# Performance work log

Measured on AMD Instinct MI355X. Metric: run time of the kernel, lower is better.

The kernel has to match this reference:

```python
import jax, jax.numpy as jnp
import numpy as np

B = 4096
DIM = 2048
B1 = 25   # root children (level-2 inner nodes)
B2 = 40   # leaves per level-2 node
NUM_CLASSES = B1 * B2  # 1000


def setup_inputs() -> dict:
    key = jax.random.key(0)
    k1, k2, k3, k4 = jax.random.split(key, 4)
    x = jax.random.normal(k1, (B, DIM), dtype=jnp.float32)
    labels = jax.random.randint(k2, (B,), 0, NUM_CLASSES, dtype=jnp.int64)
    # per-node Linear(dim, num_child + 1); column 0 = 'not in subtree'
    W_root = jax.random.normal(k3, (DIM, B1 + 1), dtype=jnp.float32) * 0.02
    b_root = jnp.zeros((B1 + 1,), dtype=jnp.float32)
    W_lvl2 = jax.random.normal(k4, (B1, DIM, B2 + 1), dtype=jnp.float32) * 0.02
    b_lvl2 = jnp.zeros((B1, B2 + 1), dtype=jnp.float32)
    return {"x": x, "labels": labels, "W_root": W_root, "b_root": b_root,
            "W_lvl2": W_lvl2, "b_lvl2": b_lvl2}


def reference(x, labels, W_root, b_root, W_lvl2, b_lvl2):
    b = x.shape[0]
    b1 = W_lvl2.shape[0]
    b2 = W_lvl2.shape[2] - 1

    # layer 1: root classifier (root.path_prob == 1.0)
    root_logits = x @ W_root + b_root                       # [B, b1+1]
    root_lp = jax.nn.log_softmax(root_logits, axis=-1)
    root_prob = jnp.exp(root_lp)

    # layer 2: all level-2 node classifiers as one grouped GEMM
    lvl2_logits = jnp.einsum('bd,ndk->bnk', x, W_lvl2) + b_lvl2  # [B, b1, b2+1]
    lvl2_lp = jax.nn.log_softmax(lvl2_logits, axis=-1)
    lvl2_prob = jnp.exp(lvl2_lp)

    # leaf path_prob = P(child under node n) * P(node n under root);
    # leaves tile out columns contiguously (label2id of complete tree)
    out = (lvl2_prob[:, :, 1:] * root_prob[:, 1:, None]).reshape(b, b1 * b2)

    # penalty: CE at each inner node divided by its layer l
    j = labels // b2                                        # level-2 parent index
    i = labels % b2                                         # leaf index within parent
    ce_root = -jnp.take_along_axis(root_lp, (j + 1)[:, None], axis=1).mean()
    # sub-label for node n: i+1 if label's parent is n, else 0
    sub_lab = jnp.where(j[:, None] == jnp.arange(b1)[None, :], (i + 1)[:, None], 0)
    gathered = jnp.take_along_axis(lvl2_lp, sub_lab[:, :, None], axis=2)[..., 0]  # [B, b1]
    penalty = ce_root + (-gathered).mean(axis=0).sum() / 2.0

    return out, penalty
```

## Files before the change

### kernel.cpp

```cpp
#include <hip/hip_runtime.h>
#include <stdint.h>

#define TB 256

typedef __bf16 bf16x8 __attribute__((ext_vector_type(8)));
typedef float f32x4 __attribute__((ext_vector_type(4)));

#define AS1 __attribute__((address_space(1)))
#define AS3 __attribute__((address_space(3)))
#define GLOAD16(gp, lp) __builtin_amdgcn_global_load_lds( \
    (const AS1 unsigned int*)(gp), (AS3 unsigned int*)(lp), 16, 0, 0)

__device__ __forceinline__ unsigned short f2bf(float f) {
  uint32_t u = __builtin_bit_cast(uint32_t, f);
  u += 0x7fffu + ((u >> 16) & 1u);
  return (unsigned short)(u >> 16);
}

__device__ __forceinline__ void waitbar3() {
  __builtin_amdgcn_sched_barrier(0);
  asm volatile("s_waitcnt vmcnt(3) lgkmcnt(0)" ::: "memory");
  __builtin_amdgcn_s_barrier();
  __builtin_amdgcn_sched_barrier(0);
}
__device__ __forceinline__ void waitbar0() {
  __builtin_amdgcn_sched_barrier(0);
  asm volatile("s_waitcnt vmcnt(0) lgkmcnt(0)" ::: "memory");
  __builtin_amdgcn_s_barrier();
  __builtin_amdgcn_sched_barrier(0);
}

__global__ __launch_bounds__(TB) void k_prep(const float* __restrict__ x,
                                             const float* __restrict__ wl,
                                             const float* __restrict__ wr,
                                             const int* __restrict__ labraw,
                                             unsigned short* __restrict__ xbf,
                                             unsigned short* __restrict__ wlt,
                                             unsigned short* __restrict__ wrt,
                                             int* __restrict__ lab32,
                                             float* __restrict__ pengl) {
  int bid = blockIdx.x, t = threadIdx.x;
  if (bid < 4096) {
    int idx = bid * TB + t;
    const float4* xin = reinterpret_cast<const float4*>(x);
    float4 a = xin[idx * 2], b = xin[idx * 2 + 1];
    uint32_t p0 = f2bf(a.x) | ((uint32_t)f2bf(a.y) << 16);
    uint32_t p1 = f2bf(a.z) | ((uint32_t)f2bf(a.w) << 16);
    uint32_t p2 = f2bf(b.x) | ((uint32_t)f2bf(b.y) << 16);
    uint32_t p3 = f2bf(b.z) | ((uint32_t)f2bf(b.w) << 16);
    reinterpret_cast<uint4*>(xbf)[idx] = make_uint4(p0, p1, p2, p3);
  } else if (bid < 4928) {
    __shared__ float ld_f[2624];
    int b2 = bid - 4096;
    if (b2 < 800) {
      int n = b2 / 32, dt = b2 % 32, d0 = dt * 64;
      const float* src = wl + ((size_t)n * 2048 + d0) * 41;
      for (int i = 0; i < 11; i++) { int lin = t + TB * i; if (lin < 2624) ld_f[lin] = src[lin]; }
      __syncthreads();
      unsigned short* dst = wlt + (size_t)n * 48 * 2048 + d0;
      for (int i = 0; i < 12; i++) {
        int lin = t + TB * i;
        int wc = lin >> 6, d = lin & 63;
        float v = (wc < 41) ? ld_f[d * 41 + wc] : 0.f;
        dst[(size_t)wc * 2048 + d] = f2bf(v);
      }
    } else {
      int dt = b2 - 800, d0 = dt * 64;
      const float* src = wr + (size_t)d0 * 26;
      for (int i = 0; i < 7; i++) { int lin = t + TB * i; if (lin < 1664) ld_f[lin] = src[lin]; }
      __syncthreads();
      unsigned short* dst = wrt + d0;
      for (int i = 0; i < 8; i++) {
        int lin = t + TB * i;
        int wc = lin >> 6, d = lin & 63;
        float v = (wc < 26) ? ld_f[d * 26 + wc] : 0.f;
        dst[(size_t)wc * 2048 + d] = f2bf(v);
      }
    }
  } else if (bid == 4928) {
    __shared__ int orred;
    if (t == 0) { orred = 0; pengl[0] = 0.f; }
    __syncthreads();
    int acc = 0;
    for (int i = t; i < 2048; i += TB) acc |= labraw[2 * i + 1];
    atomicOr(&orred, acc);
    __syncthreads();
    bool i64 = (orred == 0);
    for (int i = t; i < 4096; i += TB) lab32[i] = i64 ? labraw[2 * i] : labraw[i];
  } else {
    int g = 25 + (bid - 4929);
    uint4* p = reinterpret_cast<uint4*>(wlt + (size_t)g * 48 * 2048);
    uint4 z = make_uint4(0, 0, 0, 0);
    for (int i = t; i < 12288; i += TB) p[i] = z;
  }
}

__global__ __launch_bounds__(512) void k_root(const unsigned short* __restrict__ xbf,
                                              const unsigned short* __restrict__ wrt,
                                              const float* __restrict__ br,
                                              const int* __restrict__ labels,
                                              float* __restrict__ rootp,
                                              float* __restrict__ pengl) {
  __shared__ __align__(16) unsigned char lds3[3][24576];
  int r0 = blockIdx.x * 16;
  int tid = threadIdx.x, lane = tid & 63, wave = tid >> 6;
  int lq = lane >> 4, lr = lane & 15;
  const unsigned short* xg = xbf + (size_t)r0 * 2048;
  f32x4 acc[2] = {};

#define STAGE_RT(lb, kk)                                                              \
  do {                                                                                \
    {                                                    \
      int row = tid >> 5, s = tid & 31;                                               \
      const unsigned short* gp = xg + (size_t)row * 2048 + (kk) + ((s ^ row) << 3);   \
      GLOAD16(gp, (lb) + (size_t)tid * 16);                                           \
    }                                                                                 \
    _Pragma("unroll")                                                                 \
    for (int i = 0; i < 2; i++) {                       \
      int idx = i * 512 + tid;                                                        \
      int wc = idx >> 5, s = idx & 31;                                                \
      const unsigned short* gp = wrt + (size_t)wc * 2048 + (kk) + ((s ^ (wc & 31)) << 3); \
      GLOAD16(gp, (lb) + 8192 + (size_t)idx * 16);                                    \
    }                                                                                 \
  } while (0)

#define COMPUTE_RT(base)                                                              \
  do {                                                                                \
    int g = (wave << 2) | lq;                      \
    bf16x8 af[2], bx;                                                                 \
    _Pragma("unroll")                                                                 \
    for (int mt = 0; mt < 2; mt++) {                                                  \
      int c = mt * 16 + lr;                                                           \
      af[mt] = *reinterpret_cast<const bf16x8*>((base) + 8192 + c * 512 + ((g ^ (c & 31)) << 4)); \
    }                                                                                 \
    bx = *reinterpret_cast<const bf16x8*>((base) + lr * 512 + ((g ^ lr) << 4));       \
    _Pragma("unroll")                                                                 \
    for (int mt = 0; mt < 2; mt++)                                                    \
      acc[mt] = __builtin_amdgcn_mfma_f32_16x16x32_bf16(af[mt], bx, acc[mt], 0, 0, 0); \
  } while (0)

  STAGE_RT(&lds3[0][0], 0);
  STAGE_RT(&lds3[1][0], 256);
  waitbar3();
  int cur = 0;
#pragma unroll 3
  for (int t = 0; t < 6; ++t) {
    int nx = cur + 2; if (nx >= 3) nx -= 3;
    STAGE_RT(&lds3[nx][0], (t + 2) * 256);
    COMPUTE_RT(&lds3[cur][0]);
    waitbar3();
    ++cur; if (cur == 3) cur = 0;
  }
  COMPUTE_RT(&lds3[cur][0]);
  waitbar0();
  ++cur; if (cur == 3) cur = 0;
  COMPUTE_RT(&lds3[cur][0]);
  __syncthreads();

  float* red = (float*)&lds3[0][0];
  int li = (wave * 64 + lane) * 8;
#pragma unroll
  for (int mt = 0; mt < 2; mt++)
#pragma unroll
    for (int r = 0; r < 4; r++) red[li + mt * 4 + r] = acc[mt][r];
  __syncthreads();
  if (wave == 0) {
    float lg[2][4];
    float m = -1e30f;
#pragma unroll
    for (int mt = 0; mt < 2; mt++)
#pragma unroll
      for (int r = 0; r < 4; r++) {
        float v = 0.f;
#pragma unroll
        for (int w = 0; w < 8; w++) v += red[(w * 64 + lane) * 8 + mt * 4 + r];
        int wc = mt * 16 + lq * 4 + r;
        v += (wc < 26) ? br[wc] : -1e30f;
        lg[mt][r] = v;
        m = fmaxf(m, v);
      }
    m = fmaxf(m, __shfl_xor(m, 16));
    m = fmaxf(m, __shfl_xor(m, 32));
    float s = 0.f;
#pragma unroll
    for (int mt = 0; mt < 2; mt++)
#pragma unroll
      for (int r = 0; r < 4; r++) s += expf(lg[mt][r] - m);
    s += __shfl_xor(s, 16);
    s += __shfl_xor(s, 32);
    float ls = logf(s);
    int b = r0 + lr;
    int lab = labels[b];
    int j = lab / 40;
    float pen = 0.f;
#pragma unroll
    for (int mt = 0; mt < 2; mt++)
#pragma unroll
      for (int r = 0; r < 4; r++) {
        int wc = mt * 16 + lq * 4 + r;
        float lp = lg[mt][r] - m - ls;
        if (wc < 26) rootp[(size_t)b * 32 + wc] = expf(lp);
        if (wc == j + 1) pen -= lp;
      }
    for (int off = 32; off; off >>= 1) pen += __shfl_down(pen, off);
    if (lane == 0) atomicAdd(pengl, pen * (1.f / 4096.f));
  }
}

__global__ __launch_bounds__(TB, 2) void k_lvl2(const unsigned short* __restrict__ xbf,
                                                const unsigned short* __restrict__ wlt,
                                                const float* __restrict__ bl,
                                                const int* __restrict__ labels,
                                                const float* __restrict__ rootp,
                                                float* __restrict__ out,
                                                float* __restrict__ pengl) {
  __shared__ __align__(16) unsigned char ldsb[2][40960];
  int bid = blockIdx.x;
  int swz = (bid & 7) * 28 + (bid >> 3);
  int rt = swz / 7, quad = swz % 7;
  int r0 = rt * 128, n0 = quad * 4;
  int tid = threadIdx.x, lane = tid & 63, wave = tid >> 6;
  int wr = wave >> 1, wc = wave & 1;
  int lq = lane >> 4, lr = lane & 15;
  f32x4 acc[6][4] = {};
  const unsigned short* xg = xbf + (size_t)r0 * 2048;
  const unsigned short* wg = wlt + (size_t)n0 * 48 * 2048;

#define STAGE_L2(lb, kk)                                                              \
  do {                                                                                \
    _Pragma("unroll")                                                                 \
    for (int i = 0; i < 4; i++) {                      \
      int idx = i * 256 + tid;                                                        \
      int row = idx >> 3, s = idx & 7;                                                \
      const unsigned short* gp = xg + (size_t)row * 2048 + (kk) + ((s ^ (row & 7)) << 3); \
      GLOAD16(gp, (lb) + (size_t)idx * 16);                                           \
    }                                                                                 \
    _Pragma("unroll")                                                                 \
    for (int i = 0; i < 6; i++) {                      \
      int idx = i * 256 + tid;                                                        \
      int wrow = idx >> 3, s = idx & 7;                                               \
      const unsigned short* gp = wg + (size_t)wrow * 2048 + (kk) + ((s ^ (wrow & 7)) << 3); \
      GLOAD16(gp, (lb) + 16384 + (size_t)idx * 16);                                   \
    }                                                                                 \
  } while (0)

#define COMPUTE_L2(base)                                                              \
  do {                                                                                \
    _Pragma("unroll")                                                                 \
    for (int ks = 0; ks < 2; ks++) {                                                  \
      int g = (ks << 2) | lq;                                                         \
      bf16x8 af[6], bx[4];                                                            \
      _Pragma("unroll")                                                               \
      for (int mt = 0; mt < 6; mt++) {                                                \
        int c = wc * 96 + mt * 16 + lr;                                               \
        af[mt] = *reinterpret_cast<const bf16x8*>((base) + 16384 + c * 128 + ((g ^ (c & 7)) << 4)); \
      }                                                                               \
      _Pragma("unroll")                                                               \
      for (int nt = 0; nt < 4; nt++) {                                                \
        int row = wr * 64 + nt * 16 + lr;                                             \
        bx[nt] = *reinterpret_cast<const bf16x8*>((base) + row * 128 + ((g ^ (row & 7)) << 4)); \
      }                                                                               \
      _Pragma("unroll")                                                               \
      for (int mt = 0; mt < 6; mt++)                                                  \
        _Pragma("unroll")                                                             \
        for (int nt = 0; nt < 4; nt++)                                                \
          acc[mt][nt] = __builtin_amdgcn_mfma_f32_16x16x32_bf16(af[mt], bx[nt], acc[mt][nt], 0, 0, 0); \
    }                                                                                 \
  } while (0)

  STAGE_L2(&ldsb[0][0], 0);
  __syncthreads();
#pragma unroll 2
  for (int t = 0; t < 32; ++t) {
    if (t < 31) STAGE_L2(&ldsb[(t + 1) & 1][0], (t + 1) * 64);
    COMPUTE_L2(&ldsb[t & 1][0]);
    __syncthreads();
  }

  float pen = 0.f;
#pragma unroll
  for (int gi = 0; gi < 2; gi++) {
    int n = n0 + 2 * wc + gi;
    bool valid = (n < 25);
    float bb[3][4];
#pragma unroll
    for (int q = 0; q < 3; q++)
#pragma unroll
      for (int r = 0; r < 4; r++) {
        int wcg = q * 16 + lq * 4 + r;
        bb[q][r] = (valid && wcg < 41) ? bl[n * 41 + wcg] : -1e30f;
      }
#pragma unroll
    for (int nt = 0; nt < 4; nt++) {
      int b = r0 + wr * 64 + nt * 16 + lr;
      float lg[3][4];
      float m = -1e30f;
#pragma unroll
      for (int q = 0; q < 3; q++)
#pragma unroll
        for (int r = 0; r < 4; r++) {
          float v = acc[gi * 3 + q][nt][r] + bb[q][r];
          lg[q][r] = v;
          m = fmaxf(m, v);
        }
      m = fmaxf(m, __shfl_xor(m, 16));
      m = fmaxf(m, __shfl_xor(m, 32));
      float s = 0.f;
#pragma unroll
      for (int q = 0; q < 3; q++)
#pragma unroll
        for (int r = 0; r < 4; r++) s += expf(lg[q][r] - m);
      s += __shfl_xor(s, 16);
      s += __shfl_xor(s, 32);
      float ls = logf(s);
      float rp = valid ? rootp[(size_t)b * 32 + (n + 1)] : 0.f;
      int lab = labels[b];
      int j = lab / 40;
      int sub = (j == n) ? (lab - j * 40 + 1) : 0;
#pragma unroll
      for (int q = 0; q < 3; q++)
#pragma unroll
        for (int r = 0; r < 4; r++) {
          int wcg = q * 16 + lq * 4 + r;
          float lp = lg[q][r] - m - ls;
          if (valid && wcg >= 1 && wcg < 41) out[(size_t)b * 1000 + n * 40 + wcg - 1] = expf(lp) * rp;
          if (valid && wcg == sub) pen -= lp;
        }
    }
  }
  for (int off = 32; off; off >>= 1) pen += __shfl_down(pen, off);
  float* red = (float*)&ldsb[0][0];
  if (lane == 0) red[wave] = pen;
  __syncthreads();
  if (tid == 0) atomicAdd(pengl, (red[0] + red[1] + red[2] + red[3]) * (1.f / 8192.f));
}

extern "C" void kernel_launch(void* const* d_in, const int* in_sizes, int n_in,
                              void* d_out, int out_size, void* d_ws, size_t ws_size,
                              hipStream_t stream) {
  const float* x = (const float*)d_in[0];
  const int* labels_raw = (const int*)d_in[1];
  const float* wroot = (const float*)d_in[2];
  const float* broot = (const float*)d_in[3];
  const float* wlvl2 = (const float*)d_in[4];
  const float* blvl2 = (const float*)d_in[5];
  float* out = (float*)d_out;
  float* pengl = out + 4096000;

  char* ws = (char*)d_ws;
  unsigned short* xbf = (unsigned short*)ws;
  unsigned short* wlt = (unsigned short*)(ws + 16777216);
  unsigned short* wrt = (unsigned short*)(ws + 22282240);
  float* rootp = (float*)(ws + 22413312);
  int* lab32 = (int*)(ws + 22937600);

  k_prep<<<4932, TB, 0, stream>>>(x, wlvl2, wroot, labels_raw, xbf, wlt, wrt, lab32, pengl);
  k_root<<<256, 512, 0, stream>>>(xbf, wrt, broot, lab32, rootp, pengl);
  k_lvl2<<<224, TB, 0, stream>>>(xbf, wlt, blvl2, lab32, rootp, out, pengl);
}
```

Measured before the change: 159.1 us.

## Pre-swizzle operands into MFMA fragment layout and load directly to registers

The prep kernel now writes x and both weight sets in a fragment-major bf16 layout, so each MFMA lane's 8-element operand is a contiguous 16-byte load. The root and level-2 GEMM kernels drop LDS staging and barriers and instead load fragments straight from global memory into registers with a double-buffered register pipeline. Level-2 becomes 832 single-wave blocks, each with a 96x64 tile. This removes LDS traffic and synchronisation, at the cost of no cross-wave data sharing, so operand reuse now depends on L2 cache and register pressure is high.

```diff
diff --git a/kernel.cpp b/kernel.cpp
--- a/kernel.cpp
+++ b/kernel.cpp
@@ -5,79 +5,94 @@
 
 typedef __bf16 bf16x8 __attribute__((ext_vector_type(8)));
 typedef float f32x4 __attribute__((ext_vector_type(4)));
-
-#define AS1 __attribute__((address_space(1)))
-#define AS3 __attribute__((address_space(3)))
-#define GLOAD16(gp, lp) __builtin_amdgcn_global_load_lds( \
-    (const AS1 unsigned int*)(gp), (AS3 unsigned int*)(lp), 16, 0, 0)
 
 __device__ __forceinline__ unsigned short f2bf(float f) {
   uint32_t u = __builtin_bit_cast(uint32_t, f);
   u += 0x7fffu + ((u >> 16) & 1u);
   return (unsigned short)(u >> 16);
 }
-
-__device__ __forceinline__ void waitbar3() {
-  __builtin_amdgcn_sched_barrier(0);
-  asm volatile("s_waitcnt vmcnt(3) lgkmcnt(0)" ::: "memory");
-  __builtin_amdgcn_s_barrier();
-  __builtin_amdgcn_sched_barrier(0);
-}
-__device__ __forceinline__ void waitbar0() {
-  __builtin_amdgcn_sched_barrier(0);
-  asm volatile("s_waitcnt vmcnt(0) lgkmcnt(0)" ::: "memory");
-  __builtin_amdgcn_s_barrier();
-  __builtin_amdgcn_sched_barrier(0);
-}
+__device__ __forceinline__ uint32_t pk2(float a, float b) {
+  return (uint32_t)f2bf(a) | ((uint32_t)f2bf(b) << 16);
+}
+
+#define LD8(p) (*reinterpret_cast<const bf16x8*>(p))
+
 
 __global__ __launch_bounds__(TB) void k_prep(const float* __restrict__ x,
                                              const float* __restrict__ wl,
                                              const float* __restrict__ wr,
                                              const int* __restrict__ labraw,
-                                             unsigned short* __restrict__ xbf,
-                                             unsigned short* __restrict__ wlt,
-                                             unsigned short* __restrict__ wrt,
+                                             unsigned short* __restrict__ xf,
+                                             unsigned short* __restrict__ wf,
                                              int* __restrict__ lab32,
                                              float* __restrict__ pengl) {
+  __shared__ float ld[64 * 67];
   int bid = blockIdx.x, t = threadIdx.x;
-  if (bid < 4096) {
-    int idx = bid * TB + t;
-    const float4* xin = reinterpret_cast<const float4*>(x);
-    float4 a = xin[idx * 2], b = xin[idx * 2 + 1];
-    uint32_t p0 = f2bf(a.x) | ((uint32_t)f2bf(a.y) << 16);
-    uint32_t p1 = f2bf(a.z) | ((uint32_t)f2bf(a.w) << 16);
-    uint32_t p2 = f2bf(b.x) | ((uint32_t)f2bf(b.y) << 16);
-    uint32_t p3 = f2bf(b.z) | ((uint32_t)f2bf(b.w) << 16);
-    reinterpret_cast<uint4*>(xbf)[idx] = make_uint4(p0, p1, p2, p3);
-  } else if (bid < 4928) {
-    __shared__ float ld_f[2624];
-    int b2 = bid - 4096;
-    if (b2 < 800) {
-      int n = b2 / 32, dt = b2 % 32, d0 = dt * 64;
-      const float* src = wl + ((size_t)n * 2048 + d0) * 41;
-      for (int i = 0; i < 11; i++) { int lin = t + TB * i; if (lin < 2624) ld_f[lin] = src[lin]; }
-      __syncthreads();
-      unsigned short* dst = wlt + (size_t)n * 48 * 2048 + d0;
-      for (int i = 0; i < 12; i++) {
-        int lin = t + TB * i;
-        int wc = lin >> 6, d = lin & 63;
-        float v = (wc < 41) ? ld_f[d * 41 + wc] : 0.f;
-        dst[(size_t)wc * 2048 + d] = f2bf(v);
-      }
-    } else {
-      int dt = b2 - 800, d0 = dt * 64;
-      const float* src = wr + (size_t)d0 * 26;
-      for (int i = 0; i < 7; i++) { int lin = t + TB * i; if (lin < 1664) ld_f[lin] = src[lin]; }
-      __syncthreads();
-      unsigned short* dst = wrt + d0;
-      for (int i = 0; i < 8; i++) {
-        int lin = t + TB * i;
-        int wc = lin >> 6, d = lin & 63;
-        float v = (wc < 26) ? ld_f[d * 26 + wc] : 0.f;
-        dst[(size_t)wc * 2048 + d] = f2bf(v);
-      }
-    }
-  } else if (bid == 4928) {
+  if (bid < 2048) {
+    int rb = bid >> 5, kstep = bid & 31;
+    int r0 = rb * 64, k0 = kstep * 64;
+#pragma unroll
+    for (int u = 0; u < 4; u++) {
+      int ft = u * 256 + t;
+      int i = ft >> 4, j4 = ft & 15;
+      float4 v = *reinterpret_cast<const float4*>(x + (size_t)(r0 + i) * 2048 + k0 + j4 * 4);
+      ld[i * 67 + j4 * 4 + 0] = v.x; ld[i * 67 + j4 * 4 + 1] = v.y;
+      ld[i * 67 + j4 * 4 + 2] = v.z; ld[i * 67 + j4 * 4 + 3] = v.w;
+    }
+    __syncthreads();
+#pragma unroll
+    for (int u = 0; u < 2; u++) {
+      int c = u * 256 + t;
+      int subR = c >> 7, ks = (c >> 6) & 1, lane = c & 63;
+      int row = subR * 16 + (lane & 15);
+      int kl = ks * 32 + (lane >> 4) * 8;
+      const float* s = &ld[row * 67 + kl];
+      uint4 o = make_uint4(pk2(s[0], s[1]), pk2(s[2], s[3]), pk2(s[4], s[5]), pk2(s[6], s[7]));
+      size_t R = rb * 4 + subR;
+      *reinterpret_cast<uint4*>(xf + ((R * 32 + kstep) * 2 + ks) * 512 + lane * 8) = o;
+    }
+  } else if (bid < 2848) {
+    int b2 = bid - 2048;
+    int n = b2 >> 5, kstep = b2 & 31;
+    const float* src = wl + ((size_t)n * 2048 + kstep * 64) * 41;
+    for (int u = 0; u < 11; u++) { int lin = t + TB * u; if (lin < 2624) ld[lin] = src[lin]; }
+    __syncthreads();
+#pragma unroll
+    for (int u = 0; u < 2; u++) {
+      int c = u * 256 + t;
+      if (c < 384) {
+        int cq = c >> 7, ks = (c >> 6) & 1, lane = c & 63;
+        int col = cq * 16 + (lane & 15);
+        int kl = ks * 32 + (lane >> 4) * 8;
+        float v[8];
+#pragma unroll
+        for (int j = 0; j < 8; j++) v[j] = (col < 41) ? ld[(kl + j) * 41 + col] : 0.f;
+        uint4 o = make_uint4(pk2(v[0], v[1]), pk2(v[2], v[3]), pk2(v[4], v[5]), pk2(v[6], v[7]));
+        size_t C = n * 3 + cq;
+        *reinterpret_cast<uint4*>(wf + ((C * 32 + kstep) * 2 + ks) * 512 + lane * 8) = o;
+      }
+    }
+  } else if (bid < 2880) {
+    int kstep = bid - 2848;
+    const float* src = wr + (size_t)kstep * 64 * 26;
+    for (int u = 0; u < 7; u++) { int lin = t + TB * u; if (lin < 1664) ld[lin] = src[lin]; }
+    __syncthreads();
+#pragma unroll
+    for (int u = 0; u < 2; u++) {
+      int c = u * 256 + t;
+      if (c < 384) {
+        int cq = c >> 7, ks = (c >> 6) & 1, lane = c & 63;
+        int col = cq * 16 + (lane & 15);
+        int kl = ks * 32 + (lane >> 4) * 8;
+        float v[8];
+#pragma unroll
+        for (int j = 0; j < 8; j++) v[j] = (col < 26) ? ld[(kl + j) * 26 + col] : 0.f;
+        uint4 o = make_uint4(pk2(v[0], v[1]), pk2(v[2], v[3]), pk2(v[4], v[5]), pk2(v[6], v[7]));
+        size_t C = 75 + cq;
+        *reinterpret_cast<uint4*>(wf + ((C * 32 + kstep) * 2 + ks) * 512 + lane * 8) = o;
+      }
+    }
+  } else {
     __shared__ int orred;
     if (t == 0) { orred = 0; pengl[0] = 0.f; }
     __syncthreads();
@@ -87,77 +102,44 @@
     __syncthreads();
     bool i64 = (orred == 0);
     for (int i = t; i < 4096; i += TB) lab32[i] = i64 ? labraw[2 * i] : labraw[i];
-  } else {
-    int g = 25 + (bid - 4929);
-    uint4* p = reinterpret_cast<uint4*>(wlt + (size_t)g * 48 * 2048);
-    uint4 z = make_uint4(0, 0, 0, 0);
-    for (int i = t; i < 12288; i += TB) p[i] = z;
-  }
-}
-
-__global__ __launch_bounds__(512) void k_root(const unsigned short* __restrict__ xbf,
-                                              const unsigned short* __restrict__ wrt,
-                                              const float* __restrict__ br,
-                                              const int* __restrict__ labels,
-                                              float* __restrict__ rootp,
-                                              float* __restrict__ pengl) {
-  __shared__ __align__(16) unsigned char lds3[3][24576];
-  int r0 = blockIdx.x * 16;
+  }
+}
+
+__global__ __launch_bounds__(TB) void k_root(const unsigned short* __restrict__ xf,
+                                             const unsigned short* __restrict__ wf,
+                                             const float* __restrict__ br,
+                                             const int* __restrict__ labels,
+                                             float* __restrict__ rootp,
+                                             float* __restrict__ pengl) {
+  __shared__ float red[4 * 64 * 8];
+  int bid = blockIdx.x;
   int tid = threadIdx.x, lane = tid & 63, wave = tid >> 6;
   int lq = lane >> 4, lr = lane & 15;
-  const unsigned short* xg = xbf + (size_t)r0 * 2048;
   f32x4 acc[2] = {};
-
-#define STAGE_RT(lb, kk)                                                              \
-  do {                                                                                \
-    {                                                    \
-      int row = tid >> 5, s = tid & 31;                                               \
-      const unsigned short* gp = xg + (size_t)row * 2048 + (kk) + ((s ^ row) << 3);   \
-      GLOAD16(gp, (lb) + (size_t)tid * 16);                                           \
-    }                                                                                 \
-    _Pragma("unroll")                                                                 \
-    for (int i = 0; i < 2; i++) {                       \
-      int idx = i * 512 + tid;                                                        \
-      int wc = idx >> 5, s = idx & 31;                                                \
-      const unsigned short* gp = wrt + (size_t)wc * 2048 + (kk) + ((s ^ (wc & 31)) << 3); \
-      GLOAD16(gp, (lb) + 8192 + (size_t)idx * 16);                                    \
-    }                                                                                 \
-  } while (0)
-
-#define COMPUTE_RT(base)                                                              \
-  do {                                                                                \
-    int g = (wave << 2) | lq;                      \
-    bf16x8 af[2], bx;                                                                 \
-    _Pragma("unroll")                                                                 \
-    for (int mt = 0; mt < 2; mt++) {                                                  \
-      int c = mt * 16 + lr;                                                           \
-      af[mt] = *reinterpret_cast<const bf16x8*>((base) + 8192 + c * 512 + ((g ^ (c & 31)) << 4)); \
-    }                                                                                 \
-    bx = *reinterpret_cast<const bf16x8*>((base) + lr * 512 + ((g ^ lr) << 4));       \
-    _Pragma("unroll")                                                                 \
-    for (int mt = 0; mt < 2; mt++)                                                    \
-      acc[mt] = __builtin_amdgcn_mfma_f32_16x16x32_bf16(af[mt], bx, acc[mt], 0, 0, 0); \
-  } while (0)
-
-  STAGE_RT(&lds3[0][0], 0);
-  STAGE_RT(&lds3[1][0], 256);
-  waitbar3();
-  int cur = 0;
-#pragma unroll 3
-  for (int t = 0; t < 6; ++t) {
-    int nx = cur + 2; if (nx >= 3) nx -= 3;
-    STAGE_RT(&lds3[nx][0], (t + 2) * 256);
-    COMPUTE_RT(&lds3[cur][0]);
-    waitbar3();
-    ++cur; if (cur == 3) cur = 0;
-  }
-  COMPUTE_RT(&lds3[cur][0]);
-  waitbar0();
-  ++cur; if (cur == 3) cur = 0;
-  COMPUTE_RT(&lds3[cur][0]);
-  __syncthreads();
-
-  float* red = (float*)&lds3[0][0];
+  const unsigned short* xb = xf + (size_t)bid * 32768 + lane * 8;
+  const unsigned short* w0 = wf + (size_t)75 * 32768 + lane * 8;
+  const unsigned short* w1 = wf + (size_t)76 * 32768 + lane * 8;
+  int kb0 = wave * 8 * 1024;
+
+#define RLOAD(W, X, kb)                                                  \
+  do { _Pragma("unroll") for (int ks = 0; ks < 2; ks++) {                \
+      W[ks][0] = LD8(w0 + (kb) + ks * 512);                              \
+      W[ks][1] = LD8(w1 + (kb) + ks * 512);                              \
+      X[ks] = LD8(xb + (kb) + ks * 512); } } while (0)
+#define RMFMA(W, X)                                                      \
+  do { _Pragma("unroll") for (int ks = 0; ks < 2; ks++)                  \
+      _Pragma("unroll") for (int mt = 0; mt < 2; mt++)                   \
+        acc[mt] = __builtin_amdgcn_mfma_f32_16x16x32_bf16(W[ks][mt], X[ks], acc[mt], 0, 0, 0); } while (0)
+
+  bf16x8 A[2][2], Xa[2], B[2][2], Xb[2];
+  RLOAD(A, Xa, kb0);
+#pragma unroll
+  for (int tt = 0; tt < 3; ++tt) {
+    RLOAD(B, Xb, kb0 + (2 * tt + 1) * 1024); RMFMA(A, Xa);
+    RLOAD(A, Xa, kb0 + (2 * tt + 2) * 1024); RMFMA(B, Xb);
+  }
+  RLOAD(B, Xb, kb0 + 7 * 1024); RMFMA(A, Xa); RMFMA(B, Xb);
+
   int li = (wave * 64 + lane) * 8;
 #pragma unroll
   for (int mt = 0; mt < 2; mt++)
@@ -173,7 +155,7 @@
       for (int r = 0; r < 4; r++) {
         float v = 0.f;
 #pragma unroll
-        for (int w = 0; w < 8; w++) v += red[(w * 64 + lane) * 8 + mt * 4 + r];
+        for (int w = 0; w < 4; w++) v += red[(w * 64 + lane) * 8 + mt * 4 + r];
         int wc = mt * 16 + lq * 4 + r;
         v += (wc < 26) ? br[wc] : -1e30f;
         lg[mt][r] = v;
@@ -189,7 +171,7 @@
     s += __shfl_xor(s, 16);
     s += __shfl_xor(s, 32);
     float ls = logf(s);
-    int b = r0 + lr;
+    int b = bid * 16 + lr;
     int lab = labels[b];
     int j = lab / 40;
     float pen = 0.f;
@@ -207,80 +189,56 @@
   }
 }
 
-__global__ __launch_bounds__(TB, 2) void k_lvl2(const unsigned short* __restrict__ xbf,
-                                                const unsigned short* __restrict__ wlt,
-                                                const float* __restrict__ bl,
-                                                const int* __restrict__ labels,
-                                                const float* __restrict__ rootp,
-                                                float* __restrict__ out,
-                                                float* __restrict__ pengl) {
-  __shared__ __align__(16) unsigned char ldsb[2][40960];
+__global__ __launch_bounds__(64) void k_lvl2(const unsigned short* __restrict__ xf,
+                                             const unsigned short* __restrict__ wf,
+                                             const float* __restrict__ bl,
+                                             const int* __restrict__ labels,
+                                             const float* __restrict__ rootp,
+                                             float* __restrict__ out,
+                                             float* __restrict__ pengl) {
   int bid = blockIdx.x;
-  int swz = (bid & 7) * 28 + (bid >> 3);
-  int rt = swz / 7, quad = swz % 7;
-  int r0 = rt * 128, n0 = quad * 4;
-  int tid = threadIdx.x, lane = tid & 63, wave = tid >> 6;
-  int wr = wave >> 1, wc = wave & 1;
+  int swz = (bid & 7) * 104 + (bid >> 3);
+  int wcb = swz / 64, rt = swz % 64;
+  int lane = threadIdx.x;
   int lq = lane >> 4, lr = lane & 15;
   f32x4 acc[6][4] = {};
-  const unsigned short* xg = xbf + (size_t)r0 * 2048;
-  const unsigned short* wg = wlt + (size_t)n0 * 48 * 2048;
-
-#define STAGE_L2(lb, kk)                                                              \
-  do {                                                                                \
-    _Pragma("unroll")                                                                 \
-    for (int i = 0; i < 4; i++) {                      \
-      int idx = i * 256 + tid;                                                        \
-      int row = idx >> 3, s = idx & 7;                                                \
-      const unsigned short* gp = xg + (size_t)row * 2048 + (kk) + ((s ^ (row & 7)) << 3); \
-      GLOAD16(gp, (lb) + (size_t)idx * 16);                                           \
-    }                                                                                 \
-    _Pragma("unroll")                                                                 \
-    for (int i = 0; i < 6; i++) {                      \
-      int idx = i * 256 + tid;                                                        \
-      int wrow = idx >> 3, s = idx & 7;                                               \
-      const unsigned short* gp = wg + (size_t)wrow * 2048 + (kk) + ((s ^ (wrow & 7)) << 3); \
-      GLOAD16(gp, (lb) + 16384 + (size_t)idx * 16);                                   \
-    }                                                                                 \
-  } while (0)
-
-#define COMPUTE_L2(base)                                                              \
-  do {                                                                                \
-    _Pragma("unroll")                                                                 \
-    for (int ks = 0; ks < 2; ks++) {                                                  \
-      int g = (ks << 2) | lq;                                                         \
-      bf16x8 af[6], bx[4];                                                            \
-      _Pragma("unroll")                                                               \
-      for (int mt = 0; mt < 6; mt++) {                                                \
-        int c = wc * 96 + mt * 16 + lr;                                               \
-        af[mt] = *reinterpret_cast<const bf16x8*>((base) + 16384 + c * 128 + ((g ^ (c & 7)) << 4)); \
-      }                                                                               \
-      _Pragma("unroll")                                                               \
-      for (int nt = 0; nt < 4; nt++) {                                                \
-        int row = wr * 64 + nt * 16 + lr;                                             \
-        bx[nt] = *reinterpret_cast<const bf16x8*>((base) + row * 128 + ((g ^ (row & 7)) << 4)); \
-      }                                                                               \
-      _Pragma("unroll")                                                               \
-      for (int mt = 0; mt < 6; mt++)                                                  \
-        _Pragma("unroll")                                                             \
-        for (int nt = 0; nt < 4; nt++)                                                \
-          acc[mt][nt] = __builtin_amdgcn_mfma_f32_16x16x32_bf16(af[mt], bx[nt], acc[mt][nt], 0, 0, 0); \
-    }                                                                                 \
-  } while (0)
-
-  STAGE_L2(&ldsb[0][0], 0);
-  __syncthreads();
-#pragma unroll 2
-  for (int t = 0; t < 32; ++t) {
-    if (t < 31) STAGE_L2(&ldsb[(t + 1) & 1][0], (t + 1) * 64);
-    COMPUTE_L2(&ldsb[t & 1][0]);
-    __syncthreads();
-  }
-
+  const unsigned short* wb[6];
+  const unsigned short* xb[4];
+#pragma unroll
+  for (int c = 0; c < 6; c++) wb[c] = wf + (size_t)(wcb * 6 + c) * 32768 + lane * 8;
+#pragma unroll
+  for (int nt = 0; nt < 4; nt++) xb[nt] = xf + (size_t)(rt * 4 + nt) * 32768 + lane * 8;
+
+#define LLOAD(W, X, kb)                                                  \
+  do { _Pragma("unroll") for (int ks = 0; ks < 2; ks++) {                \
+      _Pragma("unroll") for (int c = 0; c < 6; c++)                      \
+        W[ks][c] = LD8(wb[c] + (kb) + ks * 512);                         \
+      _Pragma("unroll") for (int nt = 0; nt < 4; nt++)                   \
+        X[ks][nt] = LD8(xb[nt] + (kb) + ks * 512); } } while (0)
+#define LMFMA(W, X)                                                      \
+  do { _Pragma("unroll") for (int ks = 0; ks < 2; ks++)                  \
+      _Pragma("unroll") for (int mt = 0; mt < 6; mt++)                   \
+        _Pragma("unroll") for (int nt = 0; nt < 4; nt++)                 \
+          acc[mt][nt] = __builtin_amdgcn_mfma_f32_16x16x32_bf16(W[ks][mt], X[ks][nt], acc[mt][nt], 0, 0, 0); } while (0)
+
+  bf16x8 A[2][6], Xa[2][4], B[2][6], Xb[2][4];
+  LLOAD(A, Xa, 0);
+#pragma unroll 1
+  for (int tt = 0; tt < 15; ++tt) {
+    LLOAD(B, Xb, (2 * tt + 1) * 1024);
+    LMFMA(A, Xa);
+    LLOAD(A, Xa, (2 * tt + 2) * 1024);
+    LMFMA(B, Xb);
+  }
+  LLOAD(B, Xb, 31 * 1024);
+  LMFMA(A, Xa);
+  LMFMA(B, Xb);
+
+  int b0 = rt * 64;
   float pen = 0.f;
 #pragma unroll
   for (int gi = 0; gi < 2; gi++) {
-    int n = n0 + 2 * wc + gi;
+    int n = wcb * 2 + gi;
     bool valid = (n < 25);
     float bb[3][4];
 #pragma unroll
@@ -292,7 +250,7 @@
       }
 #pragma unroll
     for (int nt = 0; nt < 4; nt++) {
-      int b = r0 + wr * 64 + nt * 16 + lr;
+      int b = b0 + nt * 16 + lr;
       float lg[3][4];
       float m = -1e30f;
 #pragma unroll
@@ -329,10 +287,7 @@
     }
   }
   for (int off = 32; off; off >>= 1) pen += __shfl_down(pen, off);
-  float* red = (float*)&ldsb[0][0];
-  if (lane == 0) red[wave] = pen;
-  __syncthreads();
-  if (tid == 0) atomicAdd(pengl, (red[0] + red[1] + red[2] + red[3]) * (1.f / 8192.f));
+  if (lane == 0) atomicAdd(pengl, pen * (1.f / 8192.f));
 }
 
 extern "C" void kernel_launch(void* const* d_in, const int* in_sizes, int n_in,
@@ -348,13 +303,12 @@
   float* pengl = out + 4096000;
 
   char* ws = (char*)d_ws;
-  unsigned short* xbf = (unsigned short*)ws;
-  unsigned short* wlt = (unsigned short*)(ws + 16777216);
-  unsigned short* wrt = (unsigned short*)(ws + 22282240);
-  float* rootp = (float*)(ws + 22413312);
-  int* lab32 = (int*)(ws + 22937600);
-
-  k_prep<<<4932, TB, 0, stream>>>(x, wlvl2, wroot, labels_raw, xbf, wlt, wrt, lab32, pengl);
-  k_root<<<256, 512, 0, stream>>>(xbf, wrt, broot, lab32, rootp, pengl);
-  k_lvl2<<<224, TB, 0, stream>>>(xbf, wlt, blvl2, lab32, rootp, out, pengl);
-}
+  unsigned short* xf = (unsigned short*)ws;
+  unsigned short* wf = (unsigned short*)(ws + 16777216);
+  float* rootp = (float*)(ws + 21889024);
+  int* lab32 = (int*)(ws + 22413312);
+
+  k_prep<<<2881, TB, 0, stream>>>(x, wlvl2, wroot, labels_raw, xf, wf, lab32, pengl);
+  k_root<<<256, TB, 0, stream>>>(xf, wf, broot, lab32, rootp, pengl);
+  k_lvl2<<<832, 64, 0, stream>>>(xf, wf, blvl2, lab32, rootp, out, pengl);
+}
```

After: 174.7 us. 9.8% more time.

## Merge root and level-2 GEMMs into one split-K GEMM with separate epilogue

Applied to the files above, without the earlier changes.

Packs the root weights into the same transposed bf16 weight buffer as the level-2 weights, making one 4096x1280 GEMM. It runs as 640 blocks of 128x128 tiles with a two-way K split that writes fp32 partials to workspace. A separate epilogue kernel sums the partials and computes both log-softmaxes, the output probabilities and the penalty. This removes the separate root kernel and its rootp round trip and raises block count for occupancy. In exchange it adds about 42MB of partial writes and reads, drops the double-buffered LDS pipelining, and runs the epilogue with one thread per row-node over scalar loops.

```diff
diff --git a/kernel.cpp b/kernel.cpp
--- a/kernel.cpp
+++ b/kernel.cpp
@@ -15,19 +15,6 @@
   uint32_t u = __builtin_bit_cast(uint32_t, f);
   u += 0x7fffu + ((u >> 16) & 1u);
   return (unsigned short)(u >> 16);
-}
-
-__device__ __forceinline__ void waitbar3() {
-  __builtin_amdgcn_sched_barrier(0);
-  asm volatile("s_waitcnt vmcnt(3) lgkmcnt(0)" ::: "memory");
-  __builtin_amdgcn_s_barrier();
-  __builtin_amdgcn_sched_barrier(0);
-}
-__device__ __forceinline__ void waitbar0() {
-  __builtin_amdgcn_sched_barrier(0);
-  asm volatile("s_waitcnt vmcnt(0) lgkmcnt(0)" ::: "memory");
-  __builtin_amdgcn_s_barrier();
-  __builtin_amdgcn_sched_barrier(0);
 }
 
 __global__ __launch_bounds__(TB) void k_prep(const float* __restrict__ x,
@@ -36,7 +23,6 @@
                                              const int* __restrict__ labraw,
                                              unsigned short* __restrict__ xbf,
                                              unsigned short* __restrict__ wlt,
-                                             unsigned short* __restrict__ wrt,
                                              int* __restrict__ lab32,
                                              float* __restrict__ pengl) {
   int bid = blockIdx.x, t = threadIdx.x;
@@ -44,10 +30,10 @@
     int idx = bid * TB + t;
     const float4* xin = reinterpret_cast<const float4*>(x);
     float4 a = xin[idx * 2], b = xin[idx * 2 + 1];
-    uint32_t p0 = f2bf(a.x) | ((uint32_t)f2bf(a.y) << 16);
-    uint32_t p1 = f2bf(a.z) | ((uint32_t)f2bf(a.w) << 16);
-    uint32_t p2 = f2bf(b.x) | ((uint32_t)f2bf(b.y) << 16);
-    uint32_t p3 = f2bf(b.z) | ((uint32_t)f2bf(b.w) << 16);
+    uint32_t p0 = (uint32_t)f2bf(a.x) | ((uint32_t)f2bf(a.y) << 16);
+    uint32_t p1 = (uint32_t)f2bf(a.z) | ((uint32_t)f2bf(a.w) << 16);
+    uint32_t p2 = (uint32_t)f2bf(b.x) | ((uint32_t)f2bf(b.y) << 16);
+    uint32_t p3 = (uint32_t)f2bf(b.z) | ((uint32_t)f2bf(b.w) << 16);
     reinterpret_cast<uint4*>(xbf)[idx] = make_uint4(p0, p1, p2, p3);
   } else if (bid < 4928) {
     __shared__ float ld_f[2624];
@@ -69,7 +55,7 @@
       const float* src = wr + (size_t)d0 * 26;
       for (int i = 0; i < 7; i++) { int lin = t + TB * i; if (lin < 1664) ld_f[lin] = src[lin]; }
       __syncthreads();
-      unsigned short* dst = wrt + d0;
+      unsigned short* dst = wlt + (size_t)1200 * 2048 + d0;
       for (int i = 0; i < 8; i++) {
         int lin = t + TB * i;
         int wc = lin >> 6, d = lin & 63;
@@ -78,6 +64,10 @@
       }
     }
   } else if (bid == 4928) {
+    uint4* p = reinterpret_cast<uint4*>(wlt + (size_t)1232 * 2048);
+    uint4 z = make_uint4(0, 0, 0, 0);
+    for (int i = t; i < 12288; i += TB) p[i] = z;
+  } else {
     __shared__ int orred;
     if (t == 0) { orred = 0; pengl[0] = 0.f; }
     __syncthreads();
@@ -87,252 +77,161 @@
     __syncthreads();
     bool i64 = (orred == 0);
     for (int i = t; i < 4096; i += TB) lab32[i] = i64 ? labraw[2 * i] : labraw[i];
-  } else {
-    int g = 25 + (bid - 4929);
-    uint4* p = reinterpret_cast<uint4*>(wlt + (size_t)g * 48 * 2048);
-    uint4 z = make_uint4(0, 0, 0, 0);
-    for (int i = t; i < 12288; i += TB) p[i] = z;
-  }
-}
-
-__global__ __launch_bounds__(512) void k_root(const unsigned short* __restrict__ xbf,
-                                              const unsigned short* __restrict__ wrt,
-                                              const float* __restrict__ br,
-                                              const int* __restrict__ labels,
-                                              float* __restrict__ rootp,
-                                              float* __restrict__ pengl) {
-  __shared__ __align__(16) unsigned char lds3[3][24576];
-  int r0 = blockIdx.x * 16;
+  }
+}
+
+__global__ __launch_bounds__(TB) void k_gemm(const unsigned short* __restrict__ xbf,
+                                             const unsigned short* __restrict__ wlt,
+                                             float* __restrict__ part) {
+  __shared__ __align__(16) unsigned char lds[32768];
+  int bid = blockIdx.x;
+  int ord = (bid & 7) * 80 + (bid >> 3);
+  int rt = ord / 20, rem = ord % 20;
+  int ct = rem >> 1, kh = rem & 1;
+  int r0 = rt * 128, c0 = ct * 128, k0 = kh * 1024;
   int tid = threadIdx.x, lane = tid & 63, wave = tid >> 6;
+  int wavebase = wave * 64;
+  int wr = wave >> 1, wc = wave & 1;
   int lq = lane >> 4, lr = lane & 15;
-  const unsigned short* xg = xbf + (size_t)r0 * 2048;
-  f32x4 acc[2] = {};
-
-#define STAGE_RT(lb, kk)                                                              \
+  f32x4 acc[4][4] = {};
+
+#define STAGE_G(kk)                                                                   \
   do {                                                                                \
-    {                                                    \
-      int row = tid >> 5, s = tid & 31;                                               \
-      const unsigned short* gp = xg + (size_t)row * 2048 + (kk) + ((s ^ row) << 3);   \
-      GLOAD16(gp, (lb) + (size_t)tid * 16);                                           \
+    _Pragma("unroll")                                                                 \
+    for (int i = 0; i < 4; i++) {                       \
+      int idx = i * 256 + tid;                                                        \
+      int row = idx >> 3, s = idx & 7;                                                \
+      const unsigned short* gp = xbf + (size_t)(r0 + row) * 2048 + (kk) + ((s ^ (row & 7)) << 3); \
+      GLOAD16(gp, lds + (size_t)(i * 256 + wavebase) * 16);                           \
     }                                                                                 \
     _Pragma("unroll")                                                                 \
-    for (int i = 0; i < 2; i++) {                       \
-      int idx = i * 512 + tid;                                                        \
-      int wc = idx >> 5, s = idx & 31;                                                \
-      const unsigned short* gp = wrt + (size_t)wc * 2048 + (kk) + ((s ^ (wc & 31)) << 3); \
-      GLOAD16(gp, (lb) + 8192 + (size_t)idx * 16);                                    \
+    for (int i = 0; i < 4; i++) {                       \
+      int idx = i * 256 + tid;                                                        \
+      int cl = idx >> 3, s = idx & 7;                                                 \
+      const unsigned short* gp = wlt + (size_t)(c0 + cl) * 2048 + (kk) + ((s ^ (cl & 7)) << 3); \
+      GLOAD16(gp, lds + 16384 + (size_t)(i * 256 + wavebase) * 16);                   \
     }                                                                                 \
   } while (0)
 
-#define COMPUTE_RT(base)                                                              \
-  do {                                                                                \
-    int g = (wave << 2) | lq;                      \
-    bf16x8 af[2], bx;                                                                 \
-    _Pragma("unroll")                                                                 \
-    for (int mt = 0; mt < 2; mt++) {                                                  \
-      int c = mt * 16 + lr;                                                           \
-      af[mt] = *reinterpret_cast<const bf16x8*>((base) + 8192 + c * 512 + ((g ^ (c & 31)) << 4)); \
-    }                                                                                 \
-    bx = *reinterpret_cast<const bf16x8*>((base) + lr * 512 + ((g ^ lr) << 4));       \
-    _Pragma("unroll")                                                                 \
-    for (int mt = 0; mt < 2; mt++)                                                    \
-      acc[mt] = __builtin_amdgcn_mfma_f32_16x16x32_bf16(af[mt], bx, acc[mt], 0, 0, 0); \
-  } while (0)
-
-  STAGE_RT(&lds3[0][0], 0);
-  STAGE_RT(&lds3[1][0], 256);
-  waitbar3();
-  int cur = 0;
-#pragma unroll 3
-  for (int t = 0; t < 6; ++t) {
-    int nx = cur + 2; if (nx >= 3) nx -= 3;
-    STAGE_RT(&lds3[nx][0], (t + 2) * 256);
-    COMPUTE_RT(&lds3[cur][0]);
-    waitbar3();
-    ++cur; if (cur == 3) cur = 0;
-  }
-  COMPUTE_RT(&lds3[cur][0]);
-  waitbar0();
-  ++cur; if (cur == 3) cur = 0;
-  COMPUTE_RT(&lds3[cur][0]);
+  for (int t = 0; t < 16; ++t) {
+    STAGE_G(k0 + t * 64);
+    __syncthreads();
+#pragma unroll
+    for (int ks = 0; ks < 2; ks++) {
+      int g = (ks << 2) | lq;
+      bf16x8 af[4], bx[4];
+#pragma unroll
+      for (int mt = 0; mt < 4; mt++) {
+        int c = wc * 64 + mt * 16 + lr;
+        af[mt] = *reinterpret_cast<const bf16x8*>(lds + 16384 + c * 128 + ((g ^ (c & 7)) << 4));
+      }
+#pragma unroll
+      for (int nt = 0; nt < 4; nt++) {
+        int r = wr * 64 + nt * 16 + lr;
+        bx[nt] = *reinterpret_cast<const bf16x8*>(lds + r * 128 + ((g ^ (r & 7)) << 4));
+      }
+#pragma unroll
+      for (int mt = 0; mt < 4; mt++)
+#pragma unroll
+        for (int nt = 0; nt < 4; nt++)
+          acc[mt][nt] = __builtin_amdgcn_mfma_f32_16x16x32_bf16(af[mt], bx[nt], acc[mt][nt], 0, 0, 0);
+    }
+    __syncthreads();
+  }
+
+  float* pb = part + ((size_t)kh * 4096 + r0) * 1280 + c0;
+#pragma unroll
+  for (int nt = 0; nt < 4; nt++) {
+    int row = wr * 64 + nt * 16 + lr;
+#pragma unroll
+    for (int mt = 0; mt < 4; mt++) {
+      int col = wc * 64 + mt * 16 + lq * 4;
+      *reinterpret_cast<f32x4*>(pb + (size_t)row * 1280 + col) = acc[mt][nt];
+    }
+  }
+}
+
+__global__ __launch_bounds__(512) void k_epi(const float* __restrict__ part,
+                                             const float* __restrict__ br,
+                                             const float* __restrict__ bl,
+                                             const int* __restrict__ labels,
+                                             float* __restrict__ out,
+                                             float* __restrict__ pengl) {
+  __shared__ float sum_[16 * 1280];
+  __shared__ float rpl[16 * 32];
+  __shared__ float red[8];
+  int bid = blockIdx.x, t = threadIdx.x;
+  int r0 = bid * 16;
+  const float4* p0 = reinterpret_cast<const float4*>(part + (size_t)r0 * 1280);
+  const float4* p1 = reinterpret_cast<const float4*>(part + (size_t)(4096 + r0) * 1280);
+  float4* sm4 = reinterpret_cast<float4*>(sum_);
+#pragma unroll
+  for (int i = 0; i < 10; i++) {
+    int idx = i * 512 + t;
+    float4 a = p0[idx], b = p1[idx];
+    sm4[idx] = make_float4(a.x + b.x, a.y + b.y, a.z + b.z, a.w + b.w);
+  }
   __syncthreads();
 
-  float* red = (float*)&lds3[0][0];
-  int li = (wave * 64 + lane) * 8;
-#pragma unroll
-  for (int mt = 0; mt < 2; mt++)
-#pragma unroll
-    for (int r = 0; r < 4; r++) red[li + mt * 4 + r] = acc[mt][r];
-  __syncthreads();
-  if (wave == 0) {
-    float lg[2][4];
+  float pen = 0.f;
+  if (t < 16) {
+    int row = t, b = r0 + row;
+    float lg[26];
     float m = -1e30f;
 #pragma unroll
-    for (int mt = 0; mt < 2; mt++)
-#pragma unroll
-      for (int r = 0; r < 4; r++) {
-        float v = 0.f;
-#pragma unroll
-        for (int w = 0; w < 8; w++) v += red[(w * 64 + lane) * 8 + mt * 4 + r];
-        int wc = mt * 16 + lq * 4 + r;
-        v += (wc < 26) ? br[wc] : -1e30f;
-        lg[mt][r] = v;
-        m = fmaxf(m, v);
-      }
-    m = fmaxf(m, __shfl_xor(m, 16));
-    m = fmaxf(m, __shfl_xor(m, 32));
+    for (int c = 0; c < 26; c++) { lg[c] = sum_[row * 1280 + 1200 + c] + br[c]; m = fmaxf(m, lg[c]); }
     float s = 0.f;
 #pragma unroll
-    for (int mt = 0; mt < 2; mt++)
-#pragma unroll
-      for (int r = 0; r < 4; r++) s += expf(lg[mt][r] - m);
-    s += __shfl_xor(s, 16);
-    s += __shfl_xor(s, 32);
+    for (int c = 0; c < 26; c++) s += expf(lg[c] - m);
     float ls = logf(s);
-    int b = r0 + lr;
+#pragma unroll
+    for (int c = 0; c < 26; c++) rpl[row * 32 + c] = expf(lg[c] - m - ls);
     int lab = labels[b];
     int j = lab / 40;
-    float pen = 0.f;
-#pragma unroll
-    for (int mt = 0; mt < 2; mt++)
-#pragma unroll
-      for (int r = 0; r < 4; r++) {
-        int wc = mt * 16 + lq * 4 + r;
-        float lp = lg[mt][r] - m - ls;
-        if (wc < 26) rootp[(size_t)b * 32 + wc] = expf(lp);
-        if (wc == j + 1) pen -= lp;
-      }
-    for (int off = 32; off; off >>= 1) pen += __shfl_down(pen, off);
-    if (lane == 0) atomicAdd(pengl, pen * (1.f / 4096.f));
-  }
-}
-
-__global__ __launch_bounds__(TB, 2) void k_lvl2(const unsigned short* __restrict__ xbf,
-                                                const unsigned short* __restrict__ wlt,
-                                                const float* __restrict__ bl,
-                                                const int* __restrict__ labels,
-                                                const float* __restrict__ rootp,
-                                                float* __restrict__ out,
-                                                float* __restrict__ pengl) {
-  __shared__ __align__(16) unsigned char ldsb[2][40960];
-  int bid = blockIdx.x;
-  int swz = (bid & 7) * 28 + (bid >> 3);
-  int rt = swz / 7, quad = swz % 7;
-  int r0 = rt * 128, n0 = quad * 4;
-  int tid = threadIdx.x, lane = tid & 63, wave = tid >> 6;
-  int wr = wave >> 1, wc = wave & 1;
-  int lq = lane >> 4, lr = lane & 15;
-  f32x4 acc[6][4] = {};
-  const unsigned short* xg = xbf + (size_t)r0 * 2048;
-  const unsigned short* wg = wlt + (size_t)n0 * 48 * 2048;
-
-#define STAGE_L2(lb, kk)                                                              \
-  do {                                                                                \
-    _Pragma("unroll")                                                                 \
-    for (int i = 0; i < 4; i++) {                      \
-      int idx = i * 256 + tid;                                                        \
-      int row = idx >> 3, s = idx & 7;                                                \
-      const unsigned short* gp = xg + (size_t)row * 2048 + (kk) + ((s ^ (row & 7)) << 3); \
-      GLOAD16(gp, (lb) + (size_t)idx * 16);                                           \
-    }                                                                                 \
-    _Pragma("unroll")                                                                 \
-    for (int i = 0; i < 6; i++) {                      \
-      int idx = i * 256 + tid;                                                        \
-      int wrow = idx >> 3, s = idx & 7;                                               \
-      const unsigned short* gp = wg + (size_t)wrow * 2048 + (kk) + ((s ^ (wrow & 7)) << 3); \
-      GLOAD16(gp, (lb) + 16384 + (size_t)idx * 16);                                   \
-    }                                                                                 \
-  } while (0)
-
-#define COMPUTE_L2(base)                                                              \
-  do {                                                                                \
-    _Pragma("unroll")                                                                 \
-    for (int ks = 0; ks < 2; ks++) {                                                  \
-      int g = (ks << 2) | lq;                                                         \
-      bf16x8 af[6], bx[4];                                                            \
-      _Pragma("unroll")                                                               \
-      for (int mt = 0; mt < 6; mt++) {                                                \
-        int c = wc * 96 + mt * 16 + lr;                                               \
-        af[mt] = *reinterpret_cast<const bf16x8*>((base) + 16384 + c * 128 + ((g ^ (c & 7)) << 4)); \
-      }                                                                               \
-      _Pragma("unroll")                                                               \
-      for (int nt = 0; nt < 4; nt++) {                                                \
-        int row = wr * 64 + nt * 16 + lr;                                             \
-        bx[nt] = *reinterpret_cast<const bf16x8*>((base) + row * 128 + ((g ^ (row & 7)) << 4)); \
-      }                                                                               \
-      _Pragma("unroll")                                                               \
-      for (int mt = 0; mt < 6; mt++)                                                  \
-        _Pragma("unroll")                                                             \
-        for (int nt = 0; nt < 4; nt++)                                                \
-          acc[mt][nt] = __builtin_amdgcn_mfma_f32_16x16x32_bf16(af[mt], bx[nt], acc[mt][nt], 0, 0, 0); \
-    }                                                                                 \
-  } while (0)
-
-  STAGE_L2(&ldsb[0][0], 0);
+#pragma unroll
+    for (int c = 0; c < 26; c++) if (c == j + 1) pen += 2.f * (m + ls - lg[c]);
+  }
   __syncthreads();
-#pragma unroll 2
-  for (int t = 0; t < 32; ++t) {
-    if (t < 31) STAGE_L2(&ldsb[(t + 1) & 1][0], (t + 1) * 64);
-    COMPUTE_L2(&ldsb[t & 1][0]);
-    __syncthreads();
-  }
-
-  float pen = 0.f;
-#pragma unroll
-  for (int gi = 0; gi < 2; gi++) {
-    int n = n0 + 2 * wc + gi;
-    bool valid = (n < 25);
-    float bb[3][4];
-#pragma unroll
-    for (int q = 0; q < 3; q++)
-#pragma unroll
-      for (int r = 0; r < 4; r++) {
-        int wcg = q * 16 + lq * 4 + r;
-        bb[q][r] = (valid && wcg < 41) ? bl[n * 41 + wcg] : -1e30f;
-      }
-#pragma unroll
-    for (int nt = 0; nt < 4; nt++) {
-      int b = r0 + wr * 64 + nt * 16 + lr;
-      float lg[3][4];
-      float m = -1e30f;
-#pragma unroll
-      for (int q = 0; q < 3; q++)
-#pragma unroll
-        for (int r = 0; r < 4; r++) {
-          float v = acc[gi * 3 + q][nt][r] + bb[q][r];
-          lg[q][r] = v;
-          m = fmaxf(m, v);
-        }
-      m = fmaxf(m, __shfl_xor(m, 16));
-      m = fmaxf(m, __shfl_xor(m, 32));
-      float s = 0.f;
-#pragma unroll
-      for (int q = 0; q < 3; q++)
-#pragma unroll
-        for (int r = 0; r < 4; r++) s += expf(lg[q][r] - m);
-      s += __shfl_xor(s, 16);
-      s += __shfl_xor(s, 32);
-      float ls = logf(s);
-      float rp = valid ? rootp[(size_t)b * 32 + (n + 1)] : 0.f;
-      int lab = labels[b];
-      int j = lab / 40;
-      int sub = (j == n) ? (lab - j * 40 + 1) : 0;
-#pragma unroll
-      for (int q = 0; q < 3; q++)
-#pragma unroll
-        for (int r = 0; r < 4; r++) {
-          int wcg = q * 16 + lq * 4 + r;
-          float lp = lg[q][r] - m - ls;
-          if (valid && wcg >= 1 && wcg < 41) out[(size_t)b * 1000 + n * 40 + wcg - 1] = expf(lp) * rp;
-          if (valid && wcg == sub) pen -= lp;
-        }
+
+  int row = t >> 5, n = t & 31;
+  if (n < 25) {
+    int b = r0 + row;
+    const float* sb = &sum_[row * 1280 + n * 48];
+    float lg[41];
+    float m = -1e30f;
+#pragma unroll
+    for (int c = 0; c < 41; c++) { lg[c] = sb[c] + bl[n * 41 + c]; m = fmaxf(m, lg[c]); }
+    float s = 0.f;
+#pragma unroll
+    for (int c = 0; c < 41; c++) s += expf(lg[c] - m);
+    float ls = logf(s);
+    float rp = rpl[row * 32 + n + 1];
+    int lab = labels[b];
+    int j = lab / 40;
+    int sub = (j == n) ? (lab - j * 40 + 1) : 0;
+#pragma unroll
+    for (int c = 0; c < 41; c++) if (c == sub) pen += (m + ls - lg[c]);
+    float* ob = out + (size_t)b * 1000 + n * 40;
+#pragma unroll
+    for (int jj = 0; jj < 10; jj++) {
+      float4 o;
+      o.x = expf(lg[4 * jj + 1] - m - ls) * rp;
+      o.y = expf(lg[4 * jj + 2] - m - ls) * rp;
+      o.z = expf(lg[4 * jj + 3] - m - ls) * rp;
+      o.w = expf(lg[4 * jj + 4] - m - ls) * rp;
+      *reinterpret_cast<float4*>(ob + 4 * jj) = o;
     }
   }
   for (int off = 32; off; off >>= 1) pen += __shfl_down(pen, off);
-  float* red = (float*)&ldsb[0][0];
+  int lane = t & 63, wave = t >> 6;
   if (lane == 0) red[wave] = pen;
   __syncthreads();
-  if (tid == 0) atomicAdd(pengl, (red[0] + red[1] + red[2] + red[3]) * (1.f / 8192.f));
+  if (t == 0) {
+    float tot = 0.f;
+#pragma unroll
+    for (int w = 0; w < 8; w++) tot += red[w];
+    atomicAdd(pengl, tot * (1.f / 8192.f));
+  }
 }
 
 extern "C" void kernel_launch(void* const* d_in, const int* in_sizes, int n_in,
@@ -350,11 +249,10 @@
   char* ws = (char*)d_ws;
   unsigned short* xbf = (unsigned short*)ws;
   unsigned short* wlt = (unsigned short*)(ws + 16777216);
-  unsigned short* wrt = (unsigned short*)(ws + 22282240);
-  float* rootp = (float*)(ws + 22413312);
-  int* lab32 = (int*)(ws + 22937600);
-
-  k_prep<<<4932, TB, 0, stream>>>(x, wlvl2, wroot, labels_raw, xbf, wlt, wrt, lab32, pengl);
-  k_root<<<256, 512, 0, stream>>>(xbf, wrt, broot, lab32, rootp, pengl);
-  k_lvl2<<<224, TB, 0, stream>>>(xbf, wlt, blvl2, lab32, rootp, out, pengl);
-}
+  float* part = (float*)(ws + 22020096);
+  int* lab32 = (int*)(ws + 63963136);
+
+  k_prep<<<4930, TB, 0, stream>>>(x, wlvl2, wroot, labels_raw, xbf, wlt, lab32, pengl);
+  k_gemm<<<640, TB, 0, stream>>>(xbf, wlt, part);
+  k_epi<<<256, 512, 0, stream>>>(part, broot, blvl2, lab32, out, pengl);
+}
```

Result: faster. 152.0 us (-4.4%).
